# Performance work log

Hardware: AMD Instinct MI355X
Metric: run time of the kernel (lower is better)

Reference implementation:

```python
import jax, jax.numpy as jnp
import numpy as np

B, S, D = 2, 2048, 256
H, C = 8, 32          # headNum, cDim (D == H*C)
OUT = 256             # outDim
WIN = 32              # localWindowSize (half-width)
NEG = -1e30


def setup_inputs() -> dict:
    key = jax.random.key(0)
    ks = jax.random.split(key, 9)
    scale_qk = 1.0 / np.sqrt(D)
    return {
        "Qin": jax.random.normal(ks[0], (B, S, D), jnp.float32),
        "Kin": jax.random.normal(ks[1], (B, S, D), jnp.float32),
        "Vin": jax.random.normal(ks[2], (B, S, D), jnp.float32),
        "QTrans": jax.random.normal(ks[3], (D, H * C), jnp.float32) * scale_qk,
        "KTrans": jax.random.normal(ks[4], (D, H * C), jnp.float32) * scale_qk,
        "VTrans": jax.random.normal(ks[5], (D, H * C), jnp.float32) * scale_qk,
        "GW": jax.random.normal(ks[6], (H * C, D), jnp.float32) * scale_qk,  # nn.Linear weight [out,in]
        "Gb": jnp.ones((H * C,), jnp.float32),
        "OW": jax.random.normal(ks[7], (OUT, H * C), jnp.float32) * scale_qk,
        "Ob": jnp.zeros((OUT,), jnp.float32),
    }


def reference(Qin, Kin, Vin, QTrans, KTrans, VTrans, GW, Gb, OW, Ob):
    b, s, _ = Qin.shape
    # projections -> [b, s, H, C]
    Q = (Qin @ QTrans).reshape(b, s, H, C)
    K = (Kin @ KTrans).reshape(b, s, H, C)
    V = (Vin @ VTrans).reshape(b, s, H, C)
    G = jax.nn.sigmoid(Vin @ GW.T + Gb).reshape(b, s, H, C)

    # dense scores [b, H, s, t] (matches original hnst layout with batch/head swapped)
    A = jnp.einsum('bshc,bthc->bhst', Q, K) / jnp.sqrt(jnp.asarray(C, Q.dtype))

    # whose index clamping only re-hits in-window edge positions)
    idx = jnp.arange(s)
    local = jnp.abs(idx[:, None] - idx[None, :]) <= WIN  # [s, s]
    A = jnp.where(local[None, None, :, :], A, NEG)

    A = jax.nn.softmax(A, axis=-1)

    # gated attention output: original einsum 'hnst,hnti,hnsi->nshi'
    O = jnp.einsum('bhst,bthc,bshc->bshc', A, V, G)
    return O.reshape(b, s, H * C) @ OW.T + Ob
```

## Files before the change

### kernel.cpp

```cpp
#include <hip/hip_runtime.h>
#include <hip/hip_bf16.h>

typedef __bf16 bf16_t;
typedef __attribute__((ext_vector_type(8))) __bf16 bf16x8;
typedef __attribute__((ext_vector_type(4))) __bf16 bf16x4;
typedef __attribute__((ext_vector_type(4))) float f32x4;

#define MFMA(a, b, c) __builtin_amdgcn_mfma_f32_16x16x32_bf16((a), (b), (c), 0, 0, 0)

#define WK 260

static __device__ __forceinline__ bf16x8 zero_bf16x8() {
  bf16x8 z;
#pragma unroll
  for (int i = 0; i < 8; ++i) z[i] = (bf16_t)0.f;
  return z;
}

static __device__ __forceinline__ bf16x8 join8(bf16x4 lo, bf16x4 hi) {
  bf16x8 r;
  r[0] = lo[0]; r[1] = lo[1]; r[2] = lo[2]; r[3] = lo[3];
  r[4] = hi[0]; r[5] = hi[1]; r[6] = hi[2]; r[7] = hi[3];
  return r;
}

static __device__ __forceinline__ bf16x8 cvt8(float4 a, float4 b) {
  bf16x8 r;
  r[0] = (bf16_t)a.x; r[1] = (bf16_t)a.y; r[2] = (bf16_t)a.z; r[3] = (bf16_t)a.w;
  r[4] = (bf16_t)b.x; r[5] = (bf16_t)b.y; r[6] = (bf16_t)b.z; r[7] = (bf16_t)b.w;
  return r;
}

__global__ __launch_bounds__(256) void proj_kernel(
    const float* __restrict__ Qin, const float* __restrict__ Kin,
    const float* __restrict__ Vin, const float* __restrict__ QT,
    const float* __restrict__ KT, const float* __restrict__ VTr,
    const float* __restrict__ GW, const float* __restrict__ Gb,
    const float* __restrict__ OW,
    bf16_t* __restrict__ Qb, bf16_t* __restrict__ Kb,
    bf16_t* __restrict__ VT, bf16_t* __restrict__ G,
    bf16_t* __restrict__ OWb) {
  __shared__ bf16_t Wl[128][WK];
  const int tid = threadIdx.x, w = tid >> 6, lane = tid & 63;
  const int quad = lane >> 4, t15 = lane & 15;
  const int job = blockIdx.z;

  if (job == 4) {
    if (blockIdx.y != 0 || blockIdx.x >= 4) return;
    const int base = blockIdx.x * 16384 + tid * 4;
#pragma unroll
    for (int i = 0; i < 16; ++i) {
      int idx = base + i * 1024;
      float4 v = *(const float4*)(OW + idx);
      bf16x4 o;
      o[0] = (bf16_t)v.x; o[1] = (bf16_t)v.y;
      o[2] = (bf16_t)v.z; o[3] = (bf16_t)v.w;
      *(bf16x4*)(OWb + idx) = o;
    }
    return;
  }

  const int m0 = blockIdx.x * 128 + w * 16;
  const int n0 = blockIdx.y * 128;
  const float* A = (job == 0) ? Qin : (job == 1) ? Kin : Vin;

  if (job < 3) {
    const float* src = (job == 0) ? QT : (job == 1) ? KT : VTr;
    const int nl = tid & 127;
    const int kq = (tid >> 7) * 4;
#pragma unroll 8
    for (int i = 0; i < 32; ++i) {
      int k0 = i * 8 + kq;
      float f0 = src[(size_t)(k0 + 0) * 256 + n0 + nl];
      float f1 = src[(size_t)(k0 + 1) * 256 + n0 + nl];
      float f2 = src[(size_t)(k0 + 2) * 256 + n0 + nl];
      float f3 = src[(size_t)(k0 + 3) * 256 + n0 + nl];
      bf16x4 w4;
      w4[0] = (bf16_t)f0; w4[1] = (bf16_t)f1; w4[2] = (bf16_t)f2; w4[3] = (bf16_t)f3;
      *(bf16x4*)&Wl[nl][k0] = w4;
    }
  } else {
    const int kk = (tid & 63) * 4;
    const int nw = tid >> 6;
#pragma unroll 8
    for (int i = 0; i < 32; ++i) {
      int n = i * 4 + nw;
      float4 v = *(const float4*)(GW + (size_t)(n0 + n) * 256 + kk);
      bf16x4 w4;
      w4[0] = (bf16_t)v.x; w4[1] = (bf16_t)v.y; w4[2] = (bf16_t)v.z; w4[3] = (bf16_t)v.w;
      *(bf16x4*)&Wl[n][kk] = w4;
    }
  }
  __syncthreads();

  const f32x4 zf = {0.f, 0.f, 0.f, 0.f};
  f32x4 acc[2][8];
#pragma unroll
  for (int mi = 0; mi < 2; ++mi)
#pragma unroll
    for (int nf = 0; nf < 8; ++nf) acc[mi][nf] = zf;

  for (int kc = 0; kc < 8; ++kc) {
    bf16x8 a[2];
#pragma unroll
    for (int mi = 0; mi < 2; ++mi) {
      const float* ap = A + (size_t)(m0 + mi * 64 + t15) * 256 + kc * 32 + quad * 8;
      float4 x0 = *(const float4*)ap;
      float4 x1 = *(const float4*)(ap + 4);
      a[mi] = cvt8(x0, x1);
    }
#pragma unroll
    for (int nf = 0; nf < 8; ++nf) {
      bf16x4 lo = *(const bf16x4*)&Wl[nf * 16 + t15][kc * 32 + quad * 8];
      bf16x4 hi = *(const bf16x4*)&Wl[nf * 16 + t15][kc * 32 + quad * 8 + 4];
      bf16x8 bw = join8(lo, hi);
#pragma unroll
      for (int mi = 0; mi < 2; ++mi) acc[mi][nf] = MFMA(a[mi], bw, acc[mi][nf]);
    }
  }

  if (job == 2) {
    __syncthreads();
    bf16_t* Sb = &Wl[0][0];
#pragma unroll
    for (int mi = 0; mi < 2; ++mi) {
      const int m = mi * 64 + w * 16 + quad * 4;
#pragma unroll
      for (int nf = 0; nf < 8; ++nf) {
        const int n = nf * 16 + t15;
#pragma unroll
        for (int r = 0; r < 4; ++r) Sb[n * 136 + m + r] = (bf16_t)acc[mi][nf][r];
      }
    }
    __syncthreads();
    const int mloc = (tid & 15) * 8;
    const int nl2 = tid >> 4;
    const int mg = blockIdx.x * 128 + mloc;
    const int bb = mg >> 11, s = mg & 2047;
#pragma unroll
    for (int p = 0; p < 8; ++p) {
      const int ng = n0 + p * 16 + nl2;
      const int hh = ng >> 5, c = ng & 31;
      bf16x8 v = *(const bf16x8*)&Sb[(p * 16 + nl2) * 136 + mloc];
      *(bf16x8*)(VT + (size_t)((bb * 8 + hh) * 32 + c) * 2048 + s) = v;
    }
  } else if (job == 3) {
#pragma unroll
    for (int mi = 0; mi < 2; ++mi) {
      const int mm0 = m0 + mi * 64 + quad * 4;
#pragma unroll
      for (int nf = 0; nf < 8; ++nf) {
        int nn = n0 + nf * 16 + t15;
        float bias = Gb[nn];
#pragma unroll
        for (int r = 0; r < 4; ++r) {
          float g = 1.f / (1.f + __expf(-(acc[mi][nf][r] + bias)));
          G[(size_t)(mm0 + r) * 256 + nn] = (bf16_t)g;
        }
      }
    }
  } else {
    bf16_t* dst = (job == 0) ? Qb : Kb;
#pragma unroll
    for (int mi = 0; mi < 2; ++mi) {
      const int mm0 = m0 + mi * 64 + quad * 4;
#pragma unroll
      for (int nf = 0; nf < 8; ++nf) {
        int nn = n0 + nf * 16 + t15;
#pragma unroll
        for (int r = 0; r < 4; ++r)
          dst[(size_t)(mm0 + r) * 256 + nn] = (bf16_t)acc[mi][nf][r];
      }
    }
  }
}

__global__ __launch_bounds__(512) void attn_out_kernel(
    const bf16_t* __restrict__ Qb, const bf16_t* __restrict__ Kb,
    const bf16_t* __restrict__ VT, const bf16_t* __restrict__ G,
    const bf16_t* __restrict__ OWb, const float* __restrict__ Ob,
    float* __restrict__ out) {
  __shared__ bf16_t P[8][16][104];
  __shared__ bf16_t Ol[16][WK];
  const int tid = threadIdx.x, h = tid >> 6, lane = tid & 63;
  const int quad = lane >> 4, t15 = lane & 15;
  const int bid = ((blockIdx.x & 7) << 5) | (blockIdx.x >> 3);
  const int qt = bid & 127, b = bid >> 7;
  const int q0 = qt * 16, tbase = q0 - 32;
  const size_t rowbase = (size_t)b * 2048;

  bf16x8 aq = *(const bf16x8*)(Qb + (rowbase + q0 + t15) * 256 + h * 32 + quad * 8);

  bf16x8 bv[3][2];
#pragma unroll
  for (int kc = 0; kc < 3; ++kc) {
    int ts = tbase + kc * 32 + quad * 8;
    bv[kc][0] = zero_bf16x8();
    bv[kc][1] = zero_bf16x8();
    if (ts >= 0 && ts + 8 <= 2048) {
      const bf16_t* vb = VT + ((size_t)((b * 8 + h) * 32) + t15) * 2048 + ts;
      bv[kc][0] = *(const bf16x8*)vb;
      bv[kc][1] = *(const bf16x8*)(vb + (size_t)16 * 2048);
    }
  }

  float g0[4], g1[4];
#pragma unroll
  for (int r = 0; r < 4; ++r) {
    size_t base = (rowbase + q0 + quad * 4 + r) * 256 + h * 32;
    g0[r] = (float)G[base + t15];
    g1[r] = (float)G[base + 16 + t15];
  }
  const float ob0 = Ob[h * 32 + t15];
  const float ob1 = Ob[h * 32 + 16 + t15];

  const f32x4 zf = {0.f, 0.f, 0.f, 0.f};
  f32x4 sc[5];
#pragma unroll
  for (int j = 0; j < 5; ++j) {
    int t = tbase + j * 16 + t15;
    bf16x8 bk = zero_bf16x8();
    if ((unsigned)t < 2048u)
      bk = *(const bf16x8*)(Kb + (rowbase + t) * 256 + h * 32 + quad * 8);
    sc[j] = MFMA(aq, bk, zf);
  }

  const float scale = 0.17677669529663687f;
  float mx[4] = {-3.0e38f, -3.0e38f, -3.0e38f, -3.0e38f};
#pragma unroll
  for (int j = 0; j < 5; ++j) {
    int t = tbase + j * 16 + t15;
#pragma unroll
    for (int r = 0; r < 4; ++r) {
      int q = q0 + quad * 4 + r;
      int dd = q - t;
      bool valid = ((unsigned)t < 2048u) && (dd <= 32) && (dd >= -32);
      float v = valid ? sc[j][r] * scale : -1e30f;
      sc[j][r] = v;
      mx[r] = fmaxf(mx[r], v);
    }
  }
#pragma unroll
  for (int off = 1; off < 16; off <<= 1) {
#pragma unroll
    for (int r = 0; r < 4; ++r) mx[r] = fmaxf(mx[r], __shfl_xor(mx[r], off));
  }
  float sum[4] = {0.f, 0.f, 0.f, 0.f};
#pragma unroll
  for (int j = 0; j < 5; ++j) {
#pragma unroll
    for (int r = 0; r < 4; ++r) {
      float e = __expf(sc[j][r] - mx[r]);
      sc[j][r] = e;
      sum[r] += e;
    }
  }
#pragma unroll
  for (int off = 1; off < 16; off <<= 1) {
#pragma unroll
    for (int r = 0; r < 4; ++r) sum[r] += __shfl_xor(sum[r], off);
  }
  float inv[4];
#pragma unroll
  for (int r = 0; r < 4; ++r) inv[r] = 1.f / sum[r];

#pragma unroll
  for (int j = 0; j < 5; ++j) {
#pragma unroll
    for (int r = 0; r < 4; ++r)
      P[h][quad * 4 + r][j * 16 + t15] = (bf16_t)(sc[j][r] * inv[r]);
  }
#pragma unroll
  for (int r = 0; r < 4; ++r) P[h][quad * 4 + r][80 + t15] = (bf16_t)0.f;
  __syncthreads();

  f32x4 y0 = zf, y1 = zf;
#pragma unroll
  for (int kc = 0; kc < 3; ++kc) {
    bf16x8 pa = *(const bf16x8*)&P[h][t15][kc * 32 + quad * 8];
    y0 = MFMA(pa, bv[kc][0], y0);
    y1 = MFMA(pa, bv[kc][1], y1);
  }

#pragma unroll
  for (int r = 0; r < 4; ++r) {
    Ol[quad * 4 + r][h * 32 + t15] = (bf16_t)(y0[r] * g0[r]);
    Ol[quad * 4 + r][h * 32 + 16 + t15] = (bf16_t)(y1[r] * g1[r]);
  }
  __syncthreads();

  f32x4 acc[2] = {zf, zf};
#pragma unroll
  for (int kc = 0; kc < 8; ++kc) {
    bf16x4 alo = *(const bf16x4*)&Ol[t15][kc * 32 + quad * 8];
    bf16x4 ahi = *(const bf16x4*)&Ol[t15][kc * 32 + quad * 8 + 4];
    bf16x8 a = join8(alo, ahi);
#pragma unroll
    for (int nf = 0; nf < 2; ++nf) {
      int n = h * 32 + nf * 16 + t15;
      bf16x8 w8 = *(const bf16x8*)(OWb + (size_t)n * 256 + kc * 32 + quad * 8);
      acc[nf] = MFMA(a, w8, acc[nf]);
    }
  }
#pragma unroll
  for (int nf = 0; nf < 2; ++nf) {
    int n = h * 32 + nf * 16 + t15;
    float bias = (nf == 0) ? ob0 : ob1;
#pragma unroll
    for (int r = 0; r < 4; ++r)
      out[(rowbase + q0 + quad * 4 + r) * 256 + n] = acc[nf][r] + bias;
  }
}

extern "C" void kernel_launch(void* const* d_in, const int* in_sizes, int n_in,
                              void* d_out, int out_size, void* d_ws, size_t ws_size,
                              hipStream_t stream) {
  const float* Qin = (const float*)d_in[0];
  const float* Kin = (const float*)d_in[1];
  const float* Vin = (const float*)d_in[2];
  const float* QT  = (const float*)d_in[3];
  const float* KT  = (const float*)d_in[4];
  const float* VTr = (const float*)d_in[5];
  const float* GW  = (const float*)d_in[6];
  const float* Gb  = (const float*)d_in[7];
  const float* OW  = (const float*)d_in[8];
  const float* Ob  = (const float*)d_in[9];
  float* out = (float*)d_out;

  char* ws = (char*)d_ws;
  const size_t MB = 1u << 20;
  bf16_t* Qb  = (bf16_t*)(ws + 0 * MB);
  bf16_t* Kb  = (bf16_t*)(ws + 2 * MB);
  bf16_t* VT  = (bf16_t*)(ws + 4 * MB);
  bf16_t* G   = (bf16_t*)(ws + 6 * MB);
  bf16_t* OWb = (bf16_t*)(ws + 8 * MB);

  proj_kernel<<<dim3(32, 2, 5), 256, 0, stream>>>(Qin, Kin, Vin, QT, KT, VTr,
                                                  GW, Gb, OW, Qb, Kb, VT, G, OWb);
  attn_out_kernel<<<256, 512, 0, stream>>>(Qb, Kb, VT, G, OWb, Ob, out);
}
```

Measured before the change: 101.3 us.

## Fuse projection and attention kernels with a software grid barrier

Merges the projection GEMM kernel and the local-attention/output kernel into one persistent launch of 256 blocks of 512 threads. The two phases are separated by a global atomic-counter barrier, which removes the second kernel launch and the gap between launches. The projection work is redistributed so each block computes a 128x128 tile with 8 waves, and the OW bf16 conversion is spread across all blocks. The barrier depends on all 256 blocks being resident at once and adds atomic spin cost.

```diff
diff --git a/kernel.cpp b/kernel.cpp
--- a/kernel.cpp
+++ b/kernel.cpp
@@ -9,6 +9,8 @@
 #define MFMA(a, b, c) __builtin_amdgcn_mfma_f32_16x16x32_bf16((a), (b), (c), 0, 0, 0)
 
 #define WK 260
+
+__device__ unsigned long long g_bar;
 
 static __device__ __forceinline__ bf16x8 zero_bf16x8() {
   bf16x8 z;
@@ -31,284 +33,276 @@
   return r;
 }
 
-__global__ __launch_bounds__(256) void proj_kernel(
+__global__ __launch_bounds__(512) void fused_kernel(
     const float* __restrict__ Qin, const float* __restrict__ Kin,
     const float* __restrict__ Vin, const float* __restrict__ QT,
     const float* __restrict__ KT, const float* __restrict__ VTr,
     const float* __restrict__ GW, const float* __restrict__ Gb,
-    const float* __restrict__ OW,
+    const float* __restrict__ OW, const float* __restrict__ Ob,
     bf16_t* __restrict__ Qb, bf16_t* __restrict__ Kb,
     bf16_t* __restrict__ VT, bf16_t* __restrict__ G,
-    bf16_t* __restrict__ OWb) {
-  __shared__ bf16_t Wl[128][WK];
-  const int tid = threadIdx.x, w = tid >> 6, lane = tid & 63;
+    bf16_t* __restrict__ OWb, float* __restrict__ out) {
+  __shared__ __align__(16) char smem[128 * WK * 2];
+  const int tid = threadIdx.x, lane = tid & 63;
   const int quad = lane >> 4, t15 = lane & 15;
-  const int job = blockIdx.z;
-
-  if (job == 4) {
-    if (blockIdx.y != 0 || blockIdx.x >= 4) return;
-    const int base = blockIdx.x * 16384 + tid * 4;
-#pragma unroll
-    for (int i = 0; i < 16; ++i) {
-      int idx = base + i * 1024;
-      float4 v = *(const float4*)(OW + idx);
-      bf16x4 o;
-      o[0] = (bf16_t)v.x; o[1] = (bf16_t)v.y;
-      o[2] = (bf16_t)v.z; o[3] = (bf16_t)v.w;
-      *(bf16x4*)(OWb + idx) = o;
-    }
-    return;
+  const int w = tid >> 6;
+  const int virt = ((blockIdx.x & 7) << 5) | (blockIdx.x >> 3);
+
+  if (tid < 64) {
+    const int idx = (int)blockIdx.x * 256 + tid * 4;
+    float4 v = *(const float4*)(OW + idx);
+    bf16x4 o;
+    o[0] = (bf16_t)v.x; o[1] = (bf16_t)v.y; o[2] = (bf16_t)v.z; o[3] = (bf16_t)v.w;
+    *(bf16x4*)(OWb + idx) = o;
   }
 
-  const int m0 = blockIdx.x * 128 + w * 16;
-  const int n0 = blockIdx.y * 128;
-  const float* A = (job == 0) ? Qin : (job == 1) ? Kin : Vin;
-
-  if (job < 3) {
-    const float* src = (job == 0) ? QT : (job == 1) ? KT : VTr;
-    const int nl = tid & 127;
-    const int kq = (tid >> 7) * 4;
+  {
+    const int job = virt >> 6;
+    const int ntile = (virt >> 5) & 1;
+    const int mtile = virt & 31;
+    const int m0 = mtile * 128 + w * 16;
+    const int n0 = ntile * 128;
+    const float* A = (job == 0) ? Qin : (job == 1) ? Kin : Vin;
+    bf16_t(*Wl)[WK] = (bf16_t(*)[WK])smem;
+
+    if (job < 3) {
+      const float* src = (job == 0) ? QT : (job == 1) ? KT : VTr;
+      const int nl = tid & 127;
+      const int kq = (tid >> 7) * 4;
 #pragma unroll 8
-    for (int i = 0; i < 32; ++i) {
-      int k0 = i * 8 + kq;
-      float f0 = src[(size_t)(k0 + 0) * 256 + n0 + nl];
-      float f1 = src[(size_t)(k0 + 1) * 256 + n0 + nl];
-      float f2 = src[(size_t)(k0 + 2) * 256 + n0 + nl];
-      float f3 = src[(size_t)(k0 + 3) * 256 + n0 + nl];
-      bf16x4 w4;
-      w4[0] = (bf16_t)f0; w4[1] = (bf16_t)f1; w4[2] = (bf16_t)f2; w4[3] = (bf16_t)f3;
-      *(bf16x4*)&Wl[nl][k0] = w4;
-    }
-  } else {
-    const int kk = (tid & 63) * 4;
-    const int nw = tid >> 6;
+      for (int i = 0; i < 16; ++i) {
+        int k0 = i * 16 + kq;
+        float f0 = src[(size_t)(k0 + 0) * 256 + n0 + nl];
+        float f1 = src[(size_t)(k0 + 1) * 256 + n0 + nl];
+        float f2 = src[(size_t)(k0 + 2) * 256 + n0 + nl];
+        float f3 = src[(size_t)(k0 + 3) * 256 + n0 + nl];
+        bf16x4 w4;
+        w4[0] = (bf16_t)f0; w4[1] = (bf16_t)f1; w4[2] = (bf16_t)f2; w4[3] = (bf16_t)f3;
+        *(bf16x4*)&Wl[nl][k0] = w4;
+      }
+    } else {
+      const int kk = (tid & 63) * 4;
+      const int nw = tid >> 6;
 #pragma unroll 8
-    for (int i = 0; i < 32; ++i) {
-      int n = i * 4 + nw;
-      float4 v = *(const float4*)(GW + (size_t)(n0 + n) * 256 + kk);
-      bf16x4 w4;
-      w4[0] = (bf16_t)v.x; w4[1] = (bf16_t)v.y; w4[2] = (bf16_t)v.z; w4[3] = (bf16_t)v.w;
-      *(bf16x4*)&Wl[n][kk] = w4;
-    }
-  }
-  __syncthreads();
-
-  const f32x4 zf = {0.f, 0.f, 0.f, 0.f};
-  f32x4 acc[2][8];
-#pragma unroll
-  for (int mi = 0; mi < 2; ++mi)
-#pragma unroll
-    for (int nf = 0; nf < 8; ++nf) acc[mi][nf] = zf;
-
-  for (int kc = 0; kc < 8; ++kc) {
-    bf16x8 a[2];
-#pragma unroll
-    for (int mi = 0; mi < 2; ++mi) {
-      const float* ap = A + (size_t)(m0 + mi * 64 + t15) * 256 + kc * 32 + quad * 8;
+      for (int i = 0; i < 16; ++i) {
+        int n = i * 8 + nw;
+        float4 v = *(const float4*)(GW + (size_t)(n0 + n) * 256 + kk);
+        bf16x4 w4;
+        w4[0] = (bf16_t)v.x; w4[1] = (bf16_t)v.y; w4[2] = (bf16_t)v.z; w4[3] = (bf16_t)v.w;
+        *(bf16x4*)&Wl[n][kk] = w4;
+      }
+    }
+    __syncthreads();
+
+    const f32x4 zf = {0.f, 0.f, 0.f, 0.f};
+    f32x4 acc[8];
+#pragma unroll
+    for (int nf = 0; nf < 8; ++nf) acc[nf] = zf;
+
+    for (int kc = 0; kc < 8; ++kc) {
+      const float* ap = A + (size_t)(m0 + t15) * 256 + kc * 32 + quad * 8;
       float4 x0 = *(const float4*)ap;
       float4 x1 = *(const float4*)(ap + 4);
-      a[mi] = cvt8(x0, x1);
-    }
-#pragma unroll
-    for (int nf = 0; nf < 8; ++nf) {
-      bf16x4 lo = *(const bf16x4*)&Wl[nf * 16 + t15][kc * 32 + quad * 8];
-      bf16x4 hi = *(const bf16x4*)&Wl[nf * 16 + t15][kc * 32 + quad * 8 + 4];
-      bf16x8 bw = join8(lo, hi);
-#pragma unroll
-      for (int mi = 0; mi < 2; ++mi) acc[mi][nf] = MFMA(a[mi], bw, acc[mi][nf]);
-    }
-  }
-
-  if (job == 2) {
-    __syncthreads();
-    bf16_t* Sb = &Wl[0][0];
-#pragma unroll
-    for (int mi = 0; mi < 2; ++mi) {
-      const int m = mi * 64 + w * 16 + quad * 4;
+      bf16x8 a = cvt8(x0, x1);
 #pragma unroll
       for (int nf = 0; nf < 8; ++nf) {
-        const int n = nf * 16 + t15;
-#pragma unroll
-        for (int r = 0; r < 4; ++r) Sb[n * 136 + m + r] = (bf16_t)acc[mi][nf][r];
-      }
-    }
-    __syncthreads();
-    const int mloc = (tid & 15) * 8;
-    const int nl2 = tid >> 4;
-    const int mg = blockIdx.x * 128 + mloc;
-    const int bb = mg >> 11, s = mg & 2047;
-#pragma unroll
-    for (int p = 0; p < 8; ++p) {
-      const int ng = n0 + p * 16 + nl2;
-      const int hh = ng >> 5, c = ng & 31;
-      bf16x8 v = *(const bf16x8*)&Sb[(p * 16 + nl2) * 136 + mloc];
-      *(bf16x8*)(VT + (size_t)((bb * 8 + hh) * 32 + c) * 2048 + s) = v;
-    }
-  } else if (job == 3) {
-#pragma unroll
-    for (int mi = 0; mi < 2; ++mi) {
-      const int mm0 = m0 + mi * 64 + quad * 4;
+        bf16x4 lo = *(const bf16x4*)&Wl[nf * 16 + t15][kc * 32 + quad * 8];
+        bf16x4 hi = *(const bf16x4*)&Wl[nf * 16 + t15][kc * 32 + quad * 8 + 4];
+        acc[nf] = MFMA(a, join8(lo, hi), acc[nf]);
+      }
+    }
+
+    if (job == 2) {
+      __syncthreads();
+      bf16_t* Sb = (bf16_t*)smem;
+      {
+        const int m = w * 16 + quad * 4;
+#pragma unroll
+        for (int nf = 0; nf < 8; ++nf) {
+          const int n = nf * 16 + t15;
+          bf16x4 v4;
+#pragma unroll
+          for (int r = 0; r < 4; ++r) v4[r] = (bf16_t)acc[nf][r];
+          *(bf16x4*)&Sb[n * 136 + m] = v4;
+        }
+      }
+      __syncthreads();
+      const int mloc = (tid & 15) * 8;
+      const int nl2 = tid >> 4;
+      const int mg = mtile * 128 + mloc;
+      const int bb = mg >> 11, s = mg & 2047;
+#pragma unroll
+      for (int p = 0; p < 4; ++p) {
+        const int ng = n0 + p * 32 + nl2;
+        const int hh = ng >> 5, c = ng & 31;
+        bf16x8 v = *(const bf16x8*)&Sb[(p * 32 + nl2) * 136 + mloc];
+        *(bf16x8*)(VT + (size_t)((bb * 8 + hh) * 32 + c) * 2048 + s) = v;
+      }
+    } else if (job == 3) {
+      const int mm0 = m0 + quad * 4;
 #pragma unroll
       for (int nf = 0; nf < 8; ++nf) {
         int nn = n0 + nf * 16 + t15;
         float bias = Gb[nn];
 #pragma unroll
         for (int r = 0; r < 4; ++r) {
-          float g = 1.f / (1.f + __expf(-(acc[mi][nf][r] + bias)));
+          float g = 1.f / (1.f + __expf(-(acc[nf][r] + bias)));
           G[(size_t)(mm0 + r) * 256 + nn] = (bf16_t)g;
         }
       }
-    }
-  } else {
-    bf16_t* dst = (job == 0) ? Qb : Kb;
-#pragma unroll
-    for (int mi = 0; mi < 2; ++mi) {
-      const int mm0 = m0 + mi * 64 + quad * 4;
+    } else {
+      bf16_t* dst = (job == 0) ? Qb : Kb;
+      const int mm0 = m0 + quad * 4;
 #pragma unroll
       for (int nf = 0; nf < 8; ++nf) {
         int nn = n0 + nf * 16 + t15;
 #pragma unroll
         for (int r = 0; r < 4; ++r)
-          dst[(size_t)(mm0 + r) * 256 + nn] = (bf16_t)acc[mi][nf][r];
+          dst[(size_t)(mm0 + r) * 256 + nn] = (bf16_t)acc[nf][r];
       }
     }
   }
-}
-
-__global__ __launch_bounds__(512) void attn_out_kernel(
-    const bf16_t* __restrict__ Qb, const bf16_t* __restrict__ Kb,
-    const bf16_t* __restrict__ VT, const bf16_t* __restrict__ G,
-    const bf16_t* __restrict__ OWb, const float* __restrict__ Ob,
-    float* __restrict__ out) {
-  __shared__ bf16_t P[8][16][104];
-  __shared__ bf16_t Ol[16][WK];
-  const int tid = threadIdx.x, h = tid >> 6, lane = tid & 63;
-  const int quad = lane >> 4, t15 = lane & 15;
-  const int bid = ((blockIdx.x & 7) << 5) | (blockIdx.x >> 3);
-  const int qt = bid & 127, b = bid >> 7;
-  const int q0 = qt * 16, tbase = q0 - 32;
-  const size_t rowbase = (size_t)b * 2048;
-
-  bf16x8 aq = *(const bf16x8*)(Qb + (rowbase + q0 + t15) * 256 + h * 32 + quad * 8);
-
-  bf16x8 bv[3][2];
-#pragma unroll
-  for (int kc = 0; kc < 3; ++kc) {
-    int ts = tbase + kc * 32 + quad * 8;
-    bv[kc][0] = zero_bf16x8();
-    bv[kc][1] = zero_bf16x8();
-    if (ts >= 0 && ts + 8 <= 2048) {
-      const bf16_t* vb = VT + ((size_t)((b * 8 + h) * 32) + t15) * 2048 + ts;
-      bv[kc][0] = *(const bf16x8*)vb;
-      bv[kc][1] = *(const bf16x8*)(vb + (size_t)16 * 2048);
-    }
-  }
-
-  float g0[4], g1[4];
-#pragma unroll
-  for (int r = 0; r < 4; ++r) {
-    size_t base = (rowbase + q0 + quad * 4 + r) * 256 + h * 32;
-    g0[r] = (float)G[base + t15];
-    g1[r] = (float)G[base + 16 + t15];
-  }
-  const float ob0 = Ob[h * 32 + t15];
-  const float ob1 = Ob[h * 32 + 16 + t15];
-
-  const f32x4 zf = {0.f, 0.f, 0.f, 0.f};
-  f32x4 sc[5];
-#pragma unroll
-  for (int j = 0; j < 5; ++j) {
-    int t = tbase + j * 16 + t15;
-    bf16x8 bk = zero_bf16x8();
-    if ((unsigned)t < 2048u)
-      bk = *(const bf16x8*)(Kb + (rowbase + t) * 256 + h * 32 + quad * 8);
-    sc[j] = MFMA(aq, bk, zf);
-  }
-
-  const float scale = 0.17677669529663687f;
-  float mx[4] = {-3.0e38f, -3.0e38f, -3.0e38f, -3.0e38f};
-#pragma unroll
-  for (int j = 0; j < 5; ++j) {
-    int t = tbase + j * 16 + t15;
-#pragma unroll
-    for (int r = 0; r < 4; ++r) {
-      int q = q0 + quad * 4 + r;
-      int dd = q - t;
-      bool valid = ((unsigned)t < 2048u) && (dd <= 32) && (dd >= -32);
-      float v = valid ? sc[j][r] * scale : -1e30f;
-      sc[j][r] = v;
-      mx[r] = fmaxf(mx[r], v);
-    }
-  }
-#pragma unroll
-  for (int off = 1; off < 16; off <<= 1) {
-#pragma unroll
-    for (int r = 0; r < 4; ++r) mx[r] = fmaxf(mx[r], __shfl_xor(mx[r], off));
-  }
-  float sum[4] = {0.f, 0.f, 0.f, 0.f};
-#pragma unroll
-  for (int j = 0; j < 5; ++j) {
-#pragma unroll
-    for (int r = 0; r < 4; ++r) {
-      float e = __expf(sc[j][r] - mx[r]);
-      sc[j][r] = e;
-      sum[r] += e;
-    }
-  }
-#pragma unroll
-  for (int off = 1; off < 16; off <<= 1) {
-#pragma unroll
-    for (int r = 0; r < 4; ++r) sum[r] += __shfl_xor(sum[r], off);
-  }
-  float inv[4];
-#pragma unroll
-  for (int r = 0; r < 4; ++r) inv[r] = 1.f / sum[r];
-
-#pragma unroll
-  for (int j = 0; j < 5; ++j) {
-#pragma unroll
-    for (int r = 0; r < 4; ++r)
-      P[h][quad * 4 + r][j * 16 + t15] = (bf16_t)(sc[j][r] * inv[r]);
-  }
-#pragma unroll
-  for (int r = 0; r < 4; ++r) P[h][quad * 4 + r][80 + t15] = (bf16_t)0.f;
+
+  __threadfence();
   __syncthreads();
-
-  f32x4 y0 = zf, y1 = zf;
-#pragma unroll
-  for (int kc = 0; kc < 3; ++kc) {
-    bf16x8 pa = *(const bf16x8*)&P[h][t15][kc * 32 + quad * 8];
-    y0 = MFMA(pa, bv[kc][0], y0);
-    y1 = MFMA(pa, bv[kc][1], y1);
-  }
-
-#pragma unroll
-  for (int r = 0; r < 4; ++r) {
-    Ol[quad * 4 + r][h * 32 + t15] = (bf16_t)(y0[r] * g0[r]);
-    Ol[quad * 4 + r][h * 32 + 16 + t15] = (bf16_t)(y1[r] * g1[r]);
+  if (tid == 0) {
+    unsigned long long c = atomicAdd(&g_bar, 1ull);
+    unsigned long long target = (c & ~255ull) + 256ull;
+    while (__hip_atomic_load(&g_bar, __ATOMIC_RELAXED, __HIP_MEMORY_SCOPE_AGENT) < target)
+      __builtin_amdgcn_s_sleep(2);
   }
   __syncthreads();
-
-  f32x4 acc[2] = {zf, zf};
-#pragma unroll
-  for (int kc = 0; kc < 8; ++kc) {
-    bf16x4 alo = *(const bf16x4*)&Ol[t15][kc * 32 + quad * 8];
-    bf16x4 ahi = *(const bf16x4*)&Ol[t15][kc * 32 + quad * 8 + 4];
-    bf16x8 a = join8(alo, ahi);
+  __threadfence();
+
+  {
+    bf16_t(*P)[16][104] = (bf16_t(*)[16][104])smem;
+    bf16_t(*Ol)[WK] = (bf16_t(*)[WK])(smem + 8 * 16 * 104 * 2);
+    const int h = w;
+    const int qt = virt & 127, b = virt >> 7;
+    const int q0 = qt * 16, tbase = q0 - 32;
+    const size_t rowbase = (size_t)b * 2048;
+
+    bf16x8 aq = *(const bf16x8*)(Qb + (rowbase + q0 + t15) * 256 + h * 32 + quad * 8);
+
+    bf16x8 bv[3][2];
+#pragma unroll
+    for (int kc = 0; kc < 3; ++kc) {
+      int ts = tbase + kc * 32 + quad * 8;
+      bv[kc][0] = zero_bf16x8();
+      bv[kc][1] = zero_bf16x8();
+      if (ts >= 0 && ts + 8 <= 2048) {
+        const bf16_t* vb = VT + ((size_t)((b * 8 + h) * 32) + t15) * 2048 + ts;
+        bv[kc][0] = *(const bf16x8*)vb;
+        bv[kc][1] = *(const bf16x8*)(vb + (size_t)16 * 2048);
+      }
+    }
+
+    float g0[4], g1[4];
+#pragma unroll
+    for (int r = 0; r < 4; ++r) {
+      size_t base = (rowbase + q0 + quad * 4 + r) * 256 + h * 32;
+      g0[r] = (float)G[base + t15];
+      g1[r] = (float)G[base + 16 + t15];
+    }
+    const float ob0 = Ob[h * 32 + t15];
+    const float ob1 = Ob[h * 32 + 16 + t15];
+
+    const f32x4 zf = {0.f, 0.f, 0.f, 0.f};
+    f32x4 sc[5];
+#pragma unroll
+    for (int j = 0; j < 5; ++j) {
+      int t = tbase + j * 16 + t15;
+      bf16x8 bk = zero_bf16x8();
+      if ((unsigned)t < 2048u)
+        bk = *(const bf16x8*)(Kb + (rowbase + t) * 256 + h * 32 + quad * 8);
+      sc[j] = MFMA(aq, bk, zf);
+    }
+
+    const float scale = 0.17677669529663687f;
+    float mx[4] = {-3.0e38f, -3.0e38f, -3.0e38f, -3.0e38f};
+#pragma unroll
+    for (int j = 0; j < 5; ++j) {
+      int t = tbase + j * 16 + t15;
+#pragma unroll
+      for (int r = 0; r < 4; ++r) {
+        int q = q0 + quad * 4 + r;
+        int dd = q - t;
+        bool valid = ((unsigned)t < 2048u) && (dd <= 32) && (dd >= -32);
+        float v = valid ? sc[j][r] * scale : -1e30f;
+        sc[j][r] = v;
+        mx[r] = fmaxf(mx[r], v);
+      }
+    }
+#pragma unroll
+    for (int off = 1; off < 16; off <<= 1) {
+#pragma unroll
+      for (int r = 0; r < 4; ++r) mx[r] = fmaxf(mx[r], __shfl_xor(mx[r], off));
+    }
+    float sum[4] = {0.f, 0.f, 0.f, 0.f};
+#pragma unroll
+    for (int j = 0; j < 5; ++j) {
+#pragma unroll
+      for (int r = 0; r < 4; ++r) {
+        float e = __expf(sc[j][r] - mx[r]);
+        sc[j][r] = e;
+        sum[r] += e;
+      }
+    }
+#pragma unroll
+    for (int off = 1; off < 16; off <<= 1) {
+#pragma unroll
+      for (int r = 0; r < 4; ++r) sum[r] += __shfl_xor(sum[r], off);
+    }
+    float inv[4];
+#pragma unroll
+    for (int r = 0; r < 4; ++r) inv[r] = 1.f / sum[r];
+
+#pragma unroll
+    for (int j = 0; j < 5; ++j) {
+#pragma unroll
+      for (int r = 0; r < 4; ++r)
+        P[h][quad * 4 + r][j * 16 + t15] = (bf16_t)(sc[j][r] * inv[r]);
+    }
+#pragma unroll
+    for (int r = 0; r < 4; ++r) P[h][quad * 4 + r][80 + t15] = (bf16_t)0.f;
+    __syncthreads();
+
+    f32x4 y0 = zf, y1 = zf;
+#pragma unroll
+    for (int kc = 0; kc < 3; ++kc) {
+      bf16x8 pa = *(const bf16x8*)&P[h][t15][kc * 32 + quad * 8];
+      y0 = MFMA(pa, bv[kc][0], y0);
+      y1 = MFMA(pa, bv[kc][1], y1);
+    }
+
+#pragma unroll
+    for (int r = 0; r < 4; ++r) {
+      Ol[quad * 4 + r][h * 32 + t15] = (bf16_t)(y0[r] * g0[r]);
+      Ol[quad * 4 + r][h * 32 + 16 + t15] = (bf16_t)(y1[r] * g1[r]);
+    }
+    __syncthreads();
+
+    f32x4 acc2[2] = {zf, zf};
+#pragma unroll
+    for (int kc = 0; kc < 8; ++kc) {
+      bf16x4 alo = *(const bf16x4*)&Ol[t15][kc * 32 + quad * 8];
+      bf16x4 ahi = *(const bf16x4*)&Ol[t15][kc * 32 + quad * 8 + 4];
+      bf16x8 a = join8(alo, ahi);
+#pragma unroll
+      for (int nf = 0; nf < 2; ++nf) {
+        int n = h * 32 + nf * 16 + t15;
+        bf16x8 w8 = *(const bf16x8*)(OWb + (size_t)n * 256 + kc * 32 + quad * 8);
+        acc2[nf] = MFMA(a, w8, acc2[nf]);
+      }
+    }
 #pragma unroll
     for (int nf = 0; nf < 2; ++nf) {
       int n = h * 32 + nf * 16 + t15;
-      bf16x8 w8 = *(const bf16x8*)(OWb + (size_t)n * 256 + kc * 32 + quad * 8);
-      acc[nf] = MFMA(a, w8, acc[nf]);
-    }
-  }
-#pragma unroll
-  for (int nf = 0; nf < 2; ++nf) {
-    int n = h * 32 + nf * 16 + t15;
-    float bias = (nf == 0) ? ob0 : ob1;
-#pragma unroll
-    for (int r = 0; r < 4; ++r)
-      out[(rowbase + q0 + quad * 4 + r) * 256 + n] = acc[nf][r] + bias;
+      float bias = (nf == 0) ? ob0 : ob1;
+#pragma unroll
+      for (int r = 0; r < 4; ++r)
+        out[(rowbase + q0 + quad * 4 + r) * 256 + n] = acc2[nf][r] + bias;
+    }
   }
 }
 
@@ -335,7 +329,6 @@
   bf16_t* G   = (bf16_t*)(ws + 6 * MB);
   bf16_t* OWb = (bf16_t*)(ws + 8 * MB);
 
-  proj_kernel<<<dim3(32, 2, 5), 256, 0, stream>>>(Qin, Kin, Vin, QT, KT, VTr,
-                                                  GW, Gb, OW, Qb, Kb, VT, G, OWb);
-  attn_out_kernel<<<256, 512, 0, stream>>>(Qb, Kb, VT, G, OWb, Ob, out);
-}
+  fused_kernel<<<256, 512, 0, stream>>>(Qin, Kin, Vin, QT, KT, VTr, GW, Gb,
+                                        OW, Ob, Qb, Kb, VT, G, OWb, out);
+}
```

After: 202.0 us. 99.4% more time.
